# Kernel tuning notes

Hardware: AMD Instinct MI355X
Metric: run time of the kernel (lower is better)

## Reference

```python
import jax, jax.numpy as jnp
import numpy as np

EPS = 1e-5

def lrelu(x):
    return jnp.where(x > 0, x, 0.2 * x)

def bn(x, g, b, axes):
    # training-mode batch norm over `axes` (channel is last axis)
    m = jnp.mean(x, axis=axes, keepdims=True)
    v = jnp.var(x, axis=axes, keepdims=True)
    return g * (x - m) * jax.lax.rsqrt(v + EPS) + b

def knn_idx(x, k):
    # x: [B, N, C] -> idx of k nearest neighbors (incl. self): [B, N, k]
    xx = jnp.sum(x * x, axis=-1)                       # [B, N]
    inner = jnp.einsum('bnc,bmc->bnm', x, x)           # [B, N, N]
    neg_d = 2.0 * inner - xx[:, :, None] - xx[:, None, :]
    return jax.lax.top_k(neg_d, k)[1]

def graph_feature(x, k):
    # x: [B, N, C] -> edge features [B, N, k, 2C] = cat(x_j - x_i, x_i)
    idx = knn_idx(x, k)
    nb = jax.vmap(lambda xb, ib: xb[ib])(x, idx)       # [B, N, k, C]
    xc = jnp.broadcast_to(x[:, :, None, :], nb.shape)
    return jnp.concatenate([nb - xc, xc], axis=-1)

def edge_mlp(f, W, g, b):
    # 1x1 conv over edges + BN2d + LeakyReLU(0.2)
    h = jnp.einsum('bnkc,oc->bnko', f, W)
    return lrelu(bn(h, g, b, (0, 1, 2)))

def point_mlp(f, W, g, b):
    # 1x1 conv over points + BN1d + LeakyReLU(0.2)
    h = jnp.einsum('bnc,oc->bno', f, W)
    return lrelu(bn(h, g, b, (0, 1)))

def setup_inputs():
    key = jax.random.key(0)
    ks = jax.random.split(key, 16)
    B, N, K, E, C = 8, 4096, 20, 1024, 9
    inp = {'x': jax.random.normal(ks[0], (B, 3, N), jnp.float32), 'k': K}
    shapes = {'W1': (64, 6), 'W2': (64, 64), 'W3': (64, 128), 'W4': (64, 64),
              'W5': (64, 128), 'W6': (E, 192), 'W7': (512, 1216),
              'W8': (256, 512), 'W9': (C, 256)}
    for i, (n, s) in enumerate(shapes.items()):
        inp[n] = jax.random.normal(ks[i + 1], s, jnp.float32) * 0.05
    ch = [64, 64, 64, 64, 64, E, 512, 256]
    for i, c in enumerate(ch):
        inp['g%d' % (i + 1)] = jnp.ones((c,), jnp.float32)
        inp['b%d' % (i + 1)] = jnp.zeros((c,), jnp.float32)
    return inp

def reference(x, W1, W2, W3, W4, W5, W6, W7, W8, W9,
              g1, b1, g2, b2, g3, b3, g4, b4, g5, b5, g6, b6, g7, b7, g8, b8, k):
    xt = jnp.transpose(x, (0, 2, 1))                   # [B, N, 3]
    f = graph_feature(xt, k)                           # [B, N, k, 6]
    h = edge_mlp(f, W1, g1, b1)
    h = edge_mlp(h, W2, g2, b2)
    x1 = jnp.max(h, axis=2)                            # [B, N, 64]
    f = graph_feature(x1, k)                           # [B, N, k, 128]
    h = edge_mlp(f, W3, g3, b3)
    h = edge_mlp(h, W4, g4, b4)
    x2 = jnp.max(h, axis=2)                            # [B, N, 64]
    f = graph_feature(x2, k)
    h = edge_mlp(f, W5, g5, b5)
    x3 = jnp.max(h, axis=2)                            # [B, N, 64]
    cat = jnp.concatenate([x1, x2, x3], axis=-1)       # [B, N, 192]
    h6 = point_mlp(cat, W6, g6, b6)                    # [B, N, emb_dims]
    gmax = jnp.max(h6, axis=1, keepdims=True)          # global max pool
    gmax = jnp.broadcast_to(gmax, h6.shape)
    h = jnp.concatenate([gmax, x1, x2, x3], axis=-1)   # [B, N, 1216]
    h = point_mlp(h, W7, g7, b7)
    h = point_mlp(h, W8, g8, b8)
    # dropout is identity in eval mode
    out = jnp.einsum('bnc,oc->bno', h, W9)             # [B, N, num_classes]
    return out
```

## Files before the change

### kernel.cpp

```cpp
#include <hip/hip_runtime.h>
#include <hip/hip_bf16.h>

#define BB 8
#define NN 4096
#define KNN 20
#define NPTS (BB*NN)
#define NEDGE (NPTS*KNN)
#define TKCAP 12
#define LKN 12
#define SKN 24
#define FKN 48

typedef unsigned short u16;
typedef unsigned long long u64;
typedef __attribute__((ext_vector_type(8))) short s8v;
typedef __attribute__((ext_vector_type(4))) float f4v;

__device__ __forceinline__ float bf2f(u16 u) {
    return __uint_as_float(((unsigned)u) << 16);
}
__device__ __forceinline__ u16 f2bf_rne(float f) {
  unsigned u = __float_as_uint(f);
  unsigned rb = (u >> 16) & 1;
  u += 0x7FFFu + rb;
  return (u16)(u >> 16);
}
__device__ __forceinline__ float lrelu(float v) { return v > 0.f ? v : 0.2f * v; }
__device__ __forceinline__ double lrelu64(double v) { return v > 0.0 ? v : 0.2 * v; }

__device__ __forceinline__ u64 dkey(double v, int j) {
  u64 u = (u64)__double_as_longlong(v);
  u = (u >> 63) ? ~u : (u | 0x8000000000000000ull);
  return (u & ~0xFFFull) | (u64)(4095 - j);
}

__device__ __forceinline__ u64 skey(float v, int j) {
  unsigned s = __float_as_uint(v);
  s = (s >> 31) ? ~s : (s | 0x80000000u);
  return ((u64)s << 12) | (u64)(4095 - j);
}

template <int N>
__device__ __forceinline__ void tk_insert(u64* bk, u64 k) {
  if (k > bk[N - 1]) {
    bk[N - 1] = k;
#pragma unroll
    for (int p = N - 1; p > 0; --p) {
      if (bk[p] > bk[p - 1]) { u64 tv = bk[p]; bk[p] = bk[p - 1]; bk[p - 1] = tv; }
    }
  }
}

#define TOPK_INIT() \
  u64 bk[KNN]; \
  _Pragma("unroll") for (int p_ = 0; p_ < KNN; ++p_) bk[p_] = 0ull;

#define TOPK_INSERT(kk) do { \
    u64 k_ = (kk); \
    if (k_ > bk[KNN-1]) { \
      bk[KNN-1] = k_; \
      _Pragma("unroll") \
      for (int p_ = KNN-1; p_ > 0; --p_) { \
        if (bk[p_] > bk[p_-1]) { u64 tv_ = bk[p_]; bk[p_] = bk[p_-1]; bk[p_-1] = tv_; } \
      } \
    } \
  } while (0)

#define TKBUF_DECL() \
  u64 thr_ = 0ull; u64 cb_[TKCAP]; int cnt_ = 0;
#define TKBUF_PUSH(kk) do { \
    u64 k__ = (kk); \
    if (k__ > thr_) { cb_[cnt_] = k__; ++cnt_; } \
  } while (0)
#define TKBUF_FLUSH() do { \
    for (int l_ = 0; l_ < cnt_; ++l_) TOPK_INSERT(cb_[l_]); \
    cnt_ = 0; thr_ = bk[KNN-1]; \
  } while (0)

__global__ void det_k(const void* __restrict__ g1raw, int* __restrict__ flag) {
  const u16* u = (const u16*)g1raw;
  flag[0] = (u[0] == 0x3F80) ? 1 : 0;
}

__global__ __launch_bounds__(256) void conv_k(const void* __restrict__ src,
                                              float* __restrict__ dst, int n,
                                              const int* __restrict__ flag) {
  const int mode = flag[0];
  int i = blockIdx.x * 256 + threadIdx.x;
  const int stride = gridDim.x * 256;
  if (mode) {
    const u16* s = (const u16*)src;
    for (; i < n; i += stride) dst[i] = bf2f(s[i]);
  } else {
    const float* s = (const float*)src;
    for (; i < n; i += stride) dst[i] = s[i];
  }
}

__global__ void zero_k(double* __restrict__ p, int n) {
  int i = blockIdx.x * 256 + threadIdx.x;
  if (i < n) p[i] = 0.0;
}

__global__ __launch_bounds__(256) void knn1p_k(const float* __restrict__ x,
                                               u64* __restrict__ pkey) {
  __shared__ float sx[1024], sy[1024], sz[1024];
  __shared__ double sq[1024];
  const int b = blockIdx.x, t = threadIdx.x, seg = blockIdx.z;
  const int j0 = seg * 1024;
  const float* xb = x + b * 3 * NN;
  const int i = blockIdx.y * 256 + t;
// ... 343 lines not shown
  __syncthreads();
  if (t < 64) {
    double s = 0.0;
#pragma unroll
    for (int w = 0; w < 16; ++w) s += rPd[w][t];
    atomicAdd(&st[1024 + t], s);
  }
}

__global__ __launch_bounds__(256) void e1c_k(const float* __restrict__ x, const int* __restrict__ idx,
    const float* __restrict__ W1, const float* __restrict__ sc1, const float* __restrict__ sh1,
    const float* __restrict__ W2, const float* __restrict__ sc2, const float* __restrict__ sh2,
    float* __restrict__ x1out) {
  __shared__ float f6[80][9];
  __shared__ float h1s[80][68];
  const int t = threadIdx.x;
  const int p0 = blockIdx.x * 4;
  if (t < 80) {
    int e = p0 * KNN + t;
    int pt = e / KNN;
    int b = pt >> 12, i = pt & (NN - 1);
    int j = idx[e] & (NN - 1);
    const float* xb = x + b * 3 * NN;
    float xi0 = xb[i], xi1 = xb[NN + i], xi2 = xb[2 * NN + i];
    f6[t][0] = xb[j] - xi0; f6[t][1] = xb[NN + j] - xi1; f6[t][2] = xb[2 * NN + j] - xi2;
    f6[t][3] = xi0; f6[t][4] = xi1; f6[t][5] = xi2;
  }
  __syncthreads();
  const int c = t & 63;
  const int g4 = t >> 6;
  float w1[6];
#pragma unroll
  for (int d = 0; d < 6; ++d) w1[d] = W1[c * 6 + d];
  const float s1 = sc1[c], b1 = sh1[c];
  {
    float hk[20];
#pragma unroll
    for (int k = 0; k < 20; ++k) hk[k] = 0.f;
#pragma unroll
    for (int d = 0; d < 6; ++d) {
      float w1d = w1[d];
#pragma unroll
      for (int k = 0; k < 20; ++k) hk[k] = fmaf(f6[g4 + k * 4][d], w1d, hk[k]);
    }
#pragma unroll
    for (int k = 0; k < 20; ++k)
      h1s[g4 + k * 4][c] = lrelu(fmaf(s1, hk[k], b1));
  }
  __syncthreads();
  const float s2 = sc2[c], b2 = sh2[c];
  float acc[20];
#pragma unroll
  for (int k = 0; k < 20; ++k) acc[k] = 0.f;
  for (int d0 = 0; d0 < 64; d0 += 4) {
    float4 wv = *(const float4*)&W2[c * 64 + d0];
#pragma unroll
    for (int k = 0; k < 20; ++k) {
      float4 hv = *(const float4*)&h1s[g4 * 20 + k][d0];
      acc[k] = fmaf(hv.x, wv.x, acc[k]);
      acc[k] = fmaf(hv.y, wv.y, acc[k]);
      acc[k] = fmaf(hv.z, wv.z, acc[k]);
      acc[k] = fmaf(hv.w, wv.w, acc[k]);
    }
  }
  float m = -3.4e38f;
#pragma unroll
  for (int k = 0; k < 20; ++k) {
    float v = lrelu(fmaf(s2, acc[k], b2));
    m = fmaxf(m, v);
  }
  x1out[(p0 + g4) * 64 + c] = m;
}

__global__ void xx_k(const float* __restrict__ Xp, double* __restrict__ xx,
                     float* __restrict__ xxf) {
  const int row = blockIdx.x;
  float v = Xp[(size_t)row * 64 + threadIdx.x];
  double s = (double)v * (double)v;
#pragma unroll
  for (int o = 32; o > 0; o >>= 1) s += __shfl_down(s, o, 64);
  if (threadIdx.x == 0) { xx[row] = s; xxf[row] = (float)s; }
}

__global__ __launch_bounds__(256) void e2a_k(const float* __restrict__ xp,
                                             const int* __restrict__ idx,
                                             const float* __restrict__ W,
                                             double* __restrict__ st) {
  __shared__ float As[16][68];
  __shared__ float Ws[16][68];
  __shared__ double rPd[16][68];
  const int t = threadIdx.x;
  const int tx = t & 15, ty = t >> 4;
  const int lm = t >> 2, lk = (t & 3) * 4;
  double sL[4], qL[4];
#pragma unroll
  for (int j = 0; j < 4; ++j) { sL[j] = 0.0; qL[j] = 0.0; }
  for (int tile = 0; tile < 16; ++tile) {
    const int m0 = (blockIdx.x * 16 + tile) * 64;
    const int e = m0 + lm;
    const int grow = e / KNN;
    const int gj = ((grow >> 12) << 12) + (idx[e] & (NN - 1));
    float acc[4][4];
#pragma unroll
    for (int i = 0; i < 4; ++i)
#pragma unroll
      for (int j = 0; j < 4; ++j) acc[i][j] = 0.f;
    for (int k0 = 0; k0 < 128; k0 += 16) {
      const int c = k0 + lk;
      float4 a;
      if (c < 64) {
        float4 fj = *(const float4*)&xp[(size_t)gj * 64 + c];
        float4 fi = *(const float4*)&xp[(size_t)grow * 64 + c];
        a = make_float4(fj.x - fi.x, fj.y - fi.y, fj.z - fi.z, fj.w - fi.w);
      } else {
        a = *(const float4*)&xp[(size_t)grow * 64 + (c - 64)];
      }
      As[lk + 0][lm] = a.x; As[lk + 1][lm] = a.y;
      As[lk + 2][lm] = a.z; As[lk + 3][lm] = a.w;
      float4 wv = *(const float4*)&W[(size_t)lm * 128 + c];
      Ws[lk + 0][lm] = wv.x; Ws[lk + 1][lm] = wv.y;
      Ws[lk + 2][lm] = wv.z; Ws[lk + 3][lm] = wv.w;
      __syncthreads();
#pragma unroll
      for (int kk = 0; kk < 16; ++kk) {
        float4 a4 = *(const float4*)&As[kk][ty * 4];
        float4 b4 = *(const float4*)&Ws[kk][tx * 4];
        const float* aa = (const float*)&a4;
        const float* bb = (const float*)&b4;
#pragma unroll
        for (int i = 0; i < 4; ++i)
#pragma unroll
          for (int j = 0; j < 4; ++j)
            acc[i][j] = fmaf(aa[i], bb[j], acc[i][j]);
      }
      __syncthreads();
    }
#pragma unroll
    for (int j = 0; j < 4; ++j) {
      sL[j] += (double)acc[0][j] + (double)acc[1][j] + (double)acc[2][j] + (double)acc[3][j];
      qL[j] += (double)acc[0][j] * (double)acc[0][j] + (double)acc[1][j] * (double)acc[1][j]
             + (double)acc[2][j] * (double)acc[2][j] + (double)acc[3][j] * (double)acc[3][j];
    }
  }
#pragma unroll
  for (int j = 0; j < 4; ++j) rPd[ty][tx * 4 + j] = sL[j];
  __syncthreads();
  if (t < 64) {
    double s = 0.0;
#pragma unroll
    for (int w = 0; w < 16; ++w) s += rPd[w][t];
    atomicAdd(&st[t], s);
  }
  __syncthreads();
#pragma unroll
  for (int j = 0; j < 4; ++j) rPd[ty][tx * 4 + j] = qL[j];
  __syncthreads();
  if (t < 64) {
    double s = 0.0;
#pragma unroll
    for (int w = 0; w < 16; ++w) s += rPd[w][t];
    atomicAdd(&st[1024 + t], s);
  }
}

__global__ __launch_bounds__(256) void e2b_k(const float* __restrict__ xp,
    const int* __restrict__ idx, const float* __restrict__ W3,
    const float* __restrict__ sc3, const float* __restrict__ sh3,
    const float* __restrict__ W4, double* __restrict__ st) {
  __shared__ float As[16][68];
  __shared__ float Ws[16][68];
  __shared__ float H3[64][68];
  __shared__ float W4s[64][68];
  __shared__ double rPd[16][68];
  const int t = threadIdx.x;
  const int tx = t & 15, ty = t >> 4;
  const int lm = t >> 2, lk = (t & 3) * 4;
  for (int l = t; l < 4096; l += 256) W4s[l & 63][l >> 6] = W4[l];
  double sL[4], qL[4];
#pragma unroll
  for (int j = 0; j < 4; ++j) { sL[j] = 0.0; qL[j] = 0.0; }
  for (int tile = 0; tile < 16; ++tile) {
    const int m0 = (blockIdx.x * 16 + tile) * 64;
    const int e = m0 + lm;
    const int grow = e / KNN;
    const int gj = ((grow >> 12) << 12) + (idx[e] & (NN - 1));
    float acc1[4][4];
#pragma unroll
    for (int i = 0; i < 4; ++i)
#pragma unroll
      for (int j = 0; j < 4; ++j) acc1[i][j] = 0.f;
    for (int k0 = 0; k0 < 128; k0 += 16) {
      const int c = k0 + lk;
      float4 a;
      if (c < 64) {
        float4 fj = *(const float4*)&xp[(size_t)gj * 64 + c];
        float4 fi = *(const float4*)&xp[(size_t)grow * 64 + c];
        a = make_float4(fj.x - fi.x, fj.y - fi.y, fj.z - fi.z, fj.w - fi.w);
      } else {
        a = *(const float4*)&xp[(size_t)grow * 64 + (c - 64)];
      }
      As[lk + 0][lm] = a.x; As[lk + 1][lm] = a.y;
      As[lk + 2][lm] = a.z; As[lk + 3][lm] = a.w;
      float4 wv = *(const float4*)&W3[(size_t)lm * 128 + c];
      Ws[lk + 0][lm] = wv.x; Ws[lk + 1][lm] = wv.y;
      Ws[lk + 2][lm] = wv.z; Ws[lk + 3][lm] = wv.w;
      __syncthreads();
#pragma unroll
      for (int kk = 0; kk < 16; ++kk) {
        float4 a4 = *(const float4*)&As[kk][ty * 4];
        float4 b4 = *(const float4*)&Ws[kk][tx * 4];
        const float* aa = (const float*)&a4;
        const float* bb = (const float*)&b4;
#pragma unroll
        for (int i = 0; i < 4; ++i)
#pragma unroll
          for (int j = 0; j < 4; ++j)
            acc1[i][j] = fmaf(aa[i], bb[j], acc1[i][j]);
      }
      __syncthreads();
    }
#pragma unroll
    for (int j = 0; j < 4; ++j) {
      int c = tx * 4 + j;
      float s3 = sc3[c], b3 = sh3[c];
#pragma unroll
      for (int i = 0; i < 4; ++i)
        H3[c][ty * 4 + i] = lrelu(fmaf(s3, acc1[i][j], b3));
    }
    __syncthreads();
    float acc2[4][4];
#pragma unroll
    for (int i = 0; i < 4; ++i)
#pragma unroll
      for (int j = 0; j < 4; ++j) acc2[i][j] = 0.f;
    for (int k = 0; k < 64; ++k) {
      float4 a4 = *(const float4*)&H3[k][ty * 4];
      float4 b4 = *(const float4*)&W4s[k][tx * 4];
      const float* aa = (const float*)&a4;
      const float* bb = (const float*)&b4;
#pragma unroll
      for (int i = 0; i < 4; ++i)
#pragma unroll
        for (int j = 0; j < 4; ++j) acc2[i][j] = fmaf(aa[i], bb[j], acc2[i][j]);
    }
    __syncthreads();
#pragma unroll
    for (int j = 0; j < 4; ++j) {
      sL[j] += (double)acc2[0][j] + (double)acc2[1][j] + (double)acc2[2][j] + (double)acc2[3][j];
      qL[j] += (double)acc2[0][j] * (double)acc2[0][j] + (double)acc2[1][j] * (double)acc2[1][j]
             + (double)acc2[2][j] * (double)acc2[2][j] + (double)acc2[3][j] * (double)acc2[3][j];
    }
  }
#pragma unroll
  for (int j = 0; j < 4; ++j) rPd[ty][tx * 4 + j] = sL[j];
  __syncthreads();
  if (t < 64) {
    double s = 0.0;
#pragma unroll
    for (int w = 0; w < 16; ++w) s += rPd[w][t];
    atomicAdd(&st[t], s);
  }
  __syncthreads();
#pragma unroll
  for (int j = 0; j < 4; ++j) rPd[ty][tx * 4 + j] = qL[j];
  __syncthreads();
  if (t < 64) {
    double s = 0.0;
#pragma unroll
    for (int w = 0; w < 16; ++w) s += rPd[w][t];
    atomicAdd(&st[1024 + t], s);
  }
}

__global__ __launch_bounds__(256) void e2c_k(const float* __restrict__ xp,
    const int* __restrict__ idx, const float* __restrict__ W3,
    const float* __restrict__ sc3, const float* __restrict__ sh3,
    const float* __restrict__ W4, const float* __restrict__ sc4, const float* __restrict__ sh4,
    float* __restrict__ x2out) {
  __shared__ float fs[40][132];
  __shared__ float h3s[40][68];
  __shared__ float pmax[2][2][64];
  const int t = threadIdx.x;
  const int p0 = blockIdx.x * 2;
  for (int s = 0; s < 5; ++s) {
    int lin = s * 256 + t;
    int e = lin >> 5, v4 = lin & 31;
    int col = v4 * 4;
    int eg = p0 * KNN + e;
    int pt = p0 + e / KNN;
    int jr = ((pt >> 12) << 12) + (idx[eg] & (NN - 1));
    const float* xi = xp + (size_t)pt * 64;
    const float* xj = xp + (size_t)jr * 64;
    float4 a;
    if (col < 64) {
      float4 fj = *(const float4*)&xj[col];
      float4 fi = *(const float4*)&xi[col];
      a = make_float4(fj.x - fi.x, fj.y - fi.y, fj.z - fi.z, fj.w - fi.w);
    } else {
      a = *(const float4*)&xi[col - 64];
    }
    fs[e][col + 0] = a.x; fs[e][col + 1] = a.y; fs[e][col + 2] = a.z; fs[e][col + 3] = a.w;
  }
  __syncthreads();
  const int c = t & 63;
  const int g4 = t >> 6;
  const float s3 = sc3[c], b3 = sh3[c];
  {
    float hk[10];
#pragma unroll
    for (int k = 0; k < 10; ++k) hk[k] = 0.f;
    for (int d0 = 0; d0 < 128; d0 += 4) {
      float4 wv = *(const float4*)&W3[c * 128 + d0];
#pragma unroll
      for (int k = 0; k < 10; ++k) {
        float4 fv = *(const float4*)&fs[g4 + k * 4][d0];
        hk[k] = fmaf(fv.x, wv.x, hk[k]);
        hk[k] = fmaf(fv.y, wv.y, hk[k]);
        hk[k] = fmaf(fv.z, wv.z, hk[k]);
        hk[k] = fmaf(fv.w, wv.w, hk[k]);
      }
    }
#pragma unroll
    for (int k = 0; k < 10; ++k)
      h3s[g4 + k * 4][c] = lrelu(fmaf(s3, hk[k], b3));
  }
  __syncthreads();
  const int point = g4 & 1, khalf = g4 >> 1;
  const float s4 = sc4[c], b4 = sh4[c];
  float acc[10];
#pragma unroll
  for (int k = 0; k < 10; ++k) acc[k] = 0.f;
  for (int d0 = 0; d0 < 64; d0 += 4) {
    float4 wv = *(const float4*)&W4[c * 64 + d0];
#pragma unroll
    for (int k = 0; k < 10; ++k) {
      float4 hv = *(const float4*)&h3s[point * 20 + khalf * 10 + k][d0];
      acc[k] = fmaf(hv.x, wv.x, acc[k]);
      acc[k] = fmaf(hv.y, wv.y, acc[k]);
      acc[k] = fmaf(hv.z, wv.z, acc[k]);
      acc[k] = fmaf(hv.w, wv.w, acc[k]);
    }
  }
  float m = -3.4e38f;
#pragma unroll
  for (int k = 0; k < 10; ++k) {
    float v = lrelu(fmaf(s4, acc[k], b4));
    m = fmaxf(m, v);
  }
  pmax[khalf][point][c] = m;
  __syncthreads();
  if (t < 128) {
    int pp = t >> 6, cc = t & 63;
    x2out[(p0 + pp) * 64 + cc] = fmaxf(pmax[0][pp][cc], pmax[1][pp][cc]);
  }
}

__global__ __launch_bounds__(256) void e3c_k(const float* __restrict__ xp,
    const int* __restrict__ idx, const float* __restrict__ W5,
    const float* __restrict__ sc5, const float* __restrict__ sh5,
    float* __restrict__ x3out) {
  __shared__ float fs[80][132];
  const int t = threadIdx.x;
  const int p0 = blockIdx.x * 4;
  for (int s = 0; s < 10; ++s) {
    int lin = s * 256 + t;
    int e = lin >> 5, v4 = lin & 31;
    int col = v4 * 4;
    int eg = p0 * KNN + e;
    int pt = p0 + e / KNN;
    int jr = ((pt >> 12) << 12) + (idx[eg] & (NN - 1));
    const float* xi = xp + (size_t)pt * 64;
    const float* xj = xp + (size_t)jr * 64;
    float4 a;
    if (col < 64) {
      float4 fj = *(const float4*)&xj[col];
      float4 fi = *(const float4*)&xi[col];
      a = make_float4(fj.x - fi.x, fj.y - fi.y, fj.z - fi.z, fj.w - fi.w);
    } else {
      a = *(const float4*)&xi[col - 64];
    }
    fs[e][col + 0] = a.x; fs[e][col + 1] = a.y; fs[e][col + 2] = a.z; fs[e][col + 3] = a.w;
  }
  __syncthreads();
  const int c = t & 63;
  const int g4 = t >> 6;
  const float s5 = sc5[c], b5 = sh5[c];
  float acc[20];
#pragma unroll
  for (int k = 0; k < 20; ++k) acc[k] = 0.f;
  for (int d0 = 0; d0 < 128; d0 += 4) {
    float4 wv = *(const float4*)&W5[c * 128 + d0];
#pragma unroll
    for (int k = 0; k < 20; ++k) {
      float4 fv = *(const float4*)&fs[g4 * 20 + k][d0];
      acc[k] += fv.x * wv.x;
      acc[k] += fv.y * wv.y;
      acc[k] += fv.z * wv.z;
      acc[k] += fv.w * wv.w;
    }
  }
  float m = -3.4e38f;
#pragma unroll
  for (int k = 0; k < 20; ++k) m = fmaxf(m, lrelu(s5 * acc[k] + b5));
  x3out[(p0 + g4) * 64 + c] = m;
}

__global__ __launch_bounds__(256) void g6stats_k(
    const float* __restrict__ x1p, const float* __restrict__ x2p,
    const float* __restrict__ x3p, const float* __restrict__ W6,
    double* __restrict__ st, float* __restrict__ gpmax, float* __restrict__ gpmin) {
  __shared__ float As[16][68];
  __shared__ float Ws[16][68];
  __shared__ float rP[16][64];
  const int t = threadIdx.x;
  const int m0 = blockIdx.x * 64, n0 = blockIdx.y * 64;
  const int tx = t & 15, ty = t >> 4;
  const int lm = t >> 2, lk = (t & 3) * 4;
  const int m = m0 + lm, wn = n0 + lm;
  float acc[4][4];
#pragma unroll
  for (int i = 0; i < 4; ++i)
#pragma unroll
    for (int j = 0; j < 4; ++j) acc[i][j] = 0.f;
  for (int k0 = 0; k0 < 192; k0 += 16) {
    const int c = k0 + lk;
    const float* src = (c < 64)  ? &x1p[(size_t)m * 64 + c]
                     : (c < 128) ? &x2p[(size_t)m * 64 + (c - 64)]
                                 : &x3p[(size_t)m * 64 + (c - 128)];
    float4 av = *(const float4*)src;
    As[lk + 0][lm] = av.x; As[lk + 1][lm] = av.y;
    As[lk + 2][lm] = av.z; As[lk + 3][lm] = av.w;
    float4 wv = *(const float4*)&W6[(size_t)wn * 192 + c];
    Ws[lk + 0][lm] = wv.x; Ws[lk + 1][lm] = wv.y;
    Ws[lk + 2][lm] = wv.z; Ws[lk + 3][lm] = wv.w;
    __syncthreads();
#pragma unroll
    for (int kk = 0; kk < 16; ++kk) {
      float4 a4 = *(const float4*)&As[kk][ty * 4];
      float4 b4 = *(const float4*)&Ws[kk][tx * 4];
      const float* aa = (const float*)&a4;
      const float* bb = (const float*)&b4;
#pragma unroll
      for (int i = 0; i < 4; ++i)
#pragma unroll
        for (int j = 0; j < 4; ++j)
          acc[i][j] = fmaf(aa[i], bb[j], acc[i][j]);
    }
    __syncthreads();
  }
#pragma unroll
  for (int j = 0; j < 4; ++j)
    rP[ty][tx * 4 + j] = acc[0][j] + acc[1][j] + acc[2][j] + acc[3][j];
  __syncthreads();
  if (t < 64) {
    float ssum = 0.f;
#pragma unroll
    for (int w = 0; w < 16; ++w) ssum += rP[w][t];
    atomicAdd(&st[n0 + t], (double)ssum);
  }
  __syncthreads();
#pragma unroll
  for (int j = 0; j < 4; ++j)
    rP[ty][tx * 4 + j] = acc[0][j] * acc[0][j] + acc[1][j] * acc[1][j]
                       + acc[2][j] * acc[2][j] + acc[3][j] * acc[3][j];
  __syncthreads();
  if (t < 64) {
    float qsum = 0.f;
#pragma unroll
    for (int w = 0; w < 16; ++w) qsum += rP[w][t];
    atomicAdd(&st[1024 + n0 + t], (double)qsum);
  }
  __syncthreads();
#pragma unroll
  for (int j = 0; j < 4; ++j)
    rP[ty][tx * 4 + j] = fmaxf(fmaxf(acc[0][j], acc[1][j]), fmaxf(acc[2][j], acc[3][j]));
  __syncthreads();
  if (t < 64) {
    float mx = -3.4e38f;
#pragma unroll
    for (int w = 0; w < 16; ++w) mx = fmaxf(mx, rP[w][t]);
    gpmax[(size_t)blockIdx.x * 1024 + n0 + t] = mx;
  }
  __syncthreads();
#pragma unroll
  for (int j = 0; j < 4; ++j)
    rP[ty][tx * 4 + j] = fminf(fminf(acc[0][j], acc[1][j]), fminf(acc[2][j], acc[3][j]));
  __syncthreads();
// ... 278 lines not shown
      float4 wv = *(const float4*)&W8[(size_t)(n0 + lm) * 512 + c];
      Ws[lk + 0][lm] = wv.x; Ws[lk + 1][lm] = wv.y;
      Ws[lk + 2][lm] = wv.z; Ws[lk + 3][lm] = wv.w;
      __syncthreads();
#pragma unroll
      for (int kk = 0; kk < 16; ++kk) {
        float4 a4 = *(const float4*)&As[kk][ty * 4];
        float4 b4 = *(const float4*)&Ws[kk][tx * 4];
        const float* aa = (const float*)&a4;
        const float* bb = (const float*)&b4;
#pragma unroll
        for (int i = 0; i < 4; ++i)
#pragma unroll
          for (int j = 0; j < 4; ++j)
            acc[i][j] = fmaf(aa[i], bb[j], acc[i][j]);
      }
      __syncthreads();
    }
#pragma unroll
    for (int j = 0; j < 4; ++j) {
      int c = n0 + tx * 4 + j;
      float s8 = sc8[c], b8 = sh8[c];
#pragma unroll
      for (int i = 0; i < 4; ++i) {
        float v = lrelu(s8 * acc[i][j] + b8);
#pragma unroll
        for (int o = 0; o < 9; ++o) outp[i][o] += v * w9s[o][c];
      }
    }
  }
#pragma unroll
  for (int i = 0; i < 4; ++i)
#pragma unroll
    for (int o = 0; o < 9; ++o) rP[tx][(ty * 4 + i) * 9 + o] = outp[i][o];
  __syncthreads();
  const int mode = flag[0];
  for (int l = t; l < 576; l += 256) {
    float sum = 0.f;
#pragma unroll
    for (int w = 0; w < 16; ++w) sum += rP[w][l];
    if (mode) {
      ((__hip_bfloat16*)outp_raw)[(size_t)m0 * 9 + l] = __float2bfloat16(sum);
    } else {
      ((float*)outp_raw)[(size_t)m0 * 9 + l] = sum;
    }
  }
}

extern "C" void kernel_launch(void* const* d_in, const int* in_sizes, int n_in,
                              void* d_out, int out_size, void* d_ws, size_t ws_size,
                              hipStream_t stream) {
  (void)in_sizes; (void)out_size;
  if (n_in < 27) return;

  char* p = (char*)d_ws;
  size_t used = 0;
  auto alloc = [&](size_t bytes) {
    char* r = p;
    size_t rb = (bytes + 255) & ~(size_t)255;
    p += rb; used += rb;
    return r;
  };
  int* flag    = (int*)alloc(256);
  float* xF    = (float*)alloc((size_t)98304 * 4);
  float* W1f   = (float*)alloc((size_t)384 * 4);
  float* W2f   = (float*)alloc((size_t)4096 * 4);
  float* W3f   = (float*)alloc((size_t)8192 * 4);
  float* W4f   = (float*)alloc((size_t)4096 * 4);
  float* W5f   = (float*)alloc((size_t)8192 * 4);
  float* W6f   = (float*)alloc((size_t)196608 * 4);
  float* W7f   = (float*)alloc((size_t)622592 * 4);
  float* W8f   = (float*)alloc((size_t)131072 * 4);
  float* W9f   = (float*)alloc((size_t)2304 * 4);
  float* gF    = (float*)alloc((size_t)2112 * 4);
  float* bF    = (float*)alloc((size_t)2112 * 4);
  int* idxb    = (int*)alloc((size_t)NEDGE * 4);
  double* xx   = (double*)alloc((size_t)NPTS * 8);
  float* xxfb  = (float*)alloc((size_t)NPTS * 4);
  u16* Xhi     = (u16*)alloc((size_t)NPTS * 64 * 2);
  u16* Xlo     = (u16*)alloc((size_t)NPTS * 64 * 2);
  float* x1    = (float*)alloc((size_t)NPTS * 64 * 4);
  float* x2    = (float*)alloc((size_t)NPTS * 64 * 4);
  float* x3    = (float*)alloc((size_t)NPTS * 64 * 4);
  float* gm    = (float*)alloc((size_t)BB * 1024 * 4);
  float* gpmax = (float*)alloc((size_t)512 * 1024 * 4);
  float* gpmin = (float*)alloc((size_t)512 * 1024 * 4);
  float* gW    = (float*)alloc((size_t)4096 * 4);
  float* W7r   = (float*)alloc((size_t)98304 * 4);
  double* st   = (double*)alloc((size_t)2048 * 8);
  double* stm  = (double*)alloc((size_t)32 * 8);
  float* scb   = (float*)alloc((size_t)8 * 1024 * 4);
  float* shb   = (float*)alloc((size_t)8 * 1024 * 4);
  const int h7f32 = (ws_size >= used + (size_t)NPTS * 512 * 4 + 256) ? 1 : 0;
  void* h7 = alloc((size_t)NPTS * 512 * (h7f32 ? 4 : 2));
  if (ws_size < used) return;
  u64* pkey  = (u64*)h7;
  u64* pcand = (u64*)h7;

  det_k<<<1, 1, 0, stream>>>(d_in[11], flag);
  auto conv = [&](const void* src, float* dst, int n) {
    conv_k<<<(n + 255) / 256, 256, 0, stream>>>(src, dst, n, flag);
  };
  conv(d_in[0], xF, 98304);
  conv(d_in[2], W1f, 384);    conv(d_in[3], W2f, 4096);
  conv(d_in[4], W3f, 8192);   conv(d_in[5], W4f, 4096);
  conv(d_in[6], W5f, 8192);   conv(d_in[7], W6f, 196608);
  conv(d_in[8], W7f, 622592); conv(d_in[9], W8f, 131072);
  conv(d_in[10], W9f, 2304);
  const int gsz[8] = {64, 64, 64, 64, 64, 1024, 512, 256};
  int goff[8]; int acc_ = 0;
  for (int i = 0; i < 8; ++i) { goff[i] = acc_; acc_ += gsz[i]; }
  for (int i = 0; i < 8; ++i) {
    conv(d_in[11 + 2 * i], gF + goff[i], gsz[i]);
    conv(d_in[12 + 2 * i], bF + goff[i], gsz[i]);
  }
  wpack_k<<<384, 256, 0, stream>>>(W7f, W7r);
  auto SC = [&](int l) { return scb + (size_t)(l - 1) * 1024; };
  auto SH = [&](int l) { return shb + (size_t)(l - 1) * 1024; };
  auto G  = [&](int l) { return gF + goff[l - 1]; };
  auto Bt = [&](int l) { return bF + goff[l - 1]; };

  knn1p_k<<<dim3(BB, 16, 4), 256, 0, stream>>>(xF, pkey);
  tmerge_k<<<NPTS / 256, 256, 0, stream>>>(pkey, idxb);
  zero_k<<<1, 256, 0, stream>>>(stm, 32);
  f1mom_k<<<320, 256, 0, stream>>>(xF, idxb, stm);
  fin1_k<<<1, 64, 0, stream>>>(stm, W1f, G(1), Bt(1), SC(1), SH(1), 1.0 / NEDGE);
  zero_k<<<8, 256, 0, stream>>>(st, 2048);
  e1b_k<<<NEDGE / 1024, 256, 0, stream>>>(xF, idxb, W1f, SC(1), SH(1), W2f, st);
  fin_k<<<1, 256, 0, stream>>>(st, G(2), Bt(2), SC(2), SH(2), 64, 1.0 / NEDGE);
  e1c_k<<<NPTS / 4, 256, 0, stream>>>(xF, idxb, W1f, SC(1), SH(1), W2f, SC(2), SH(2), x1);

  xx_k<<<NPTS, 64, 0, stream>>>(x1, xx, xxfb);
  xsplit_k<<<NPTS * 64 / 256, 256, 0, stream>>>(x1, Xhi, Xlo);
  knnsm_k<<<dim3(NN / 16, BB), 256, 0, stream>>>(Xhi, Xlo, xxfb, pcand);
  resc_k<<<NPTS / 4, 256, 0, stream>>>(x1, xx, pcand, idxb);

  zero_k<<<8, 256, 0, stream>>>(st, 2048);
  e2a_k<<<NEDGE / 1024, 256, 0, stream>>>(x1, idxb, W3f, st);
  fin_k<<<1, 256, 0, stream>>>(st, G(3), Bt(3), SC(3), SH(3), 64, 1.0 / NEDGE);
  zero_k<<<8, 256, 0, stream>>>(st, 2048);
  e2b_k<<<NEDGE / 1024, 256, 0, stream>>>(x1, idxb, W3f, SC(3), SH(3), W4f, st);
  fin_k<<<1, 256, 0, stream>>>(st, G(4), Bt(4), SC(4), SH(4), 64, 1.0 / NEDGE);
  e2c_k<<<NPTS / 2, 256, 0, stream>>>(x1, idxb, W3f, SC(3), SH(3), W4f, SC(4), SH(4), x2);

  xx_k<<<NPTS, 64, 0, stream>>>(x2, xx, xxfb);
  xsplit_k<<<NPTS * 64 / 256, 256, 0, stream>>>(x2, Xhi, Xlo);
  knnsm_k<<<dim3(NN / 16, BB), 256, 0, stream>>>(Xhi, Xlo, xxfb, pcand);
  resc_k<<<NPTS / 4, 256, 0, stream>>>(x2, xx, pcand, idxb);

  zero_k<<<8, 256, 0, stream>>>(st, 2048);
  e2a_k<<<NEDGE / 1024, 256, 0, stream>>>(x2, idxb, W5f, st);
  fin_k<<<1, 256, 0, stream>>>(st, G(5), Bt(5), SC(5), SH(5), 64, 1.0 / NEDGE);
  e3c_k<<<NPTS / 4, 256, 0, stream>>>(x2, idxb, W5f, SC(5), SH(5), x3);

  zero_k<<<8, 256, 0, stream>>>(st, 2048);
  g6stats_k<<<dim3(NPTS / 64, 16), 256, 0, stream>>>(x1, x2, x3, W6f, st, gpmax, gpmin);
  fin_k<<<4, 256, 0, stream>>>(st, G(6), Bt(6), SC(6), SH(6), 1024, 1.0 / NPTS);
  gmax_red2_k<<<dim3(BB, 4), 256, 0, stream>>>(gpmax, gpmin, SC(6), SH(6), gm);

  gw_k<<<16, 256, 0, stream>>>(gm, W7f, gW);
  zero_k<<<8, 256, 0, stream>>>(st, 2048);
  if (h7f32) {
    g7stats_k<1><<<dim3(NPTS / 64, 8), 256, 0, stream>>>(x1, x2, x3, W7r, gW, h7, st);
  } else {
    g7stats_k<0><<<dim3(NPTS / 64, 8), 256, 0, stream>>>(x1, x2, x3, W7r, gW, h7, st);
  }
  fin_k<<<2, 256, 0, stream>>>(st, G(7), Bt(7), SC(7), SH(7), 512, 1.0 / NPTS);

  zero_k<<<8, 256, 0, stream>>>(st, 2048);
  if (h7f32) {
    gstats_k<4, 0, 1><<<dim3(NPTS / 64, 4), 256, 0, stream>>>(
        h7, W8f, 512, 256, nullptr, nullptr, nullptr, nullptr, SC(7), SH(7), nullptr, st);
  } else {
    gstats_k<4, 0, 0><<<dim3(NPTS / 64, 4), 256, 0, stream>>>(
        h7, W8f, 512, 256, nullptr, nullptr, nullptr, nullptr, SC(7), SH(7), nullptr, st);
  }
  fin_k<<<1, 256, 0, stream>>>(st, G(8), Bt(8), SC(8), SH(8), 256, 1.0 / NPTS);

  if (h7f32) {
    final_k<1><<<NPTS / 64, 256, 0, stream>>>(h7, SC(7), SH(7), W8f, SC(8), SH(8), W9f,
                                              d_out, flag);
  } else {
    final_k<0><<<NPTS / 64, 256, 0, stream>>>(h7, SC(7), SH(7), W8f, SC(8), SH(8), W9f,
                                              d_out, flag);
  }
}
```

Baseline: 3.781 ms.

## Factor edge conv as per-point GEMMs: W[:, :64]·x_j + (W[:, 64:]-W[:, :64])·x_i

```diff
diff --git a/kernel.cpp b/kernel.cpp
--- a/kernel.cpp
+++ b/kernel.cpp
@@ -26,7 +26,6 @@
   return (u16)(u >> 16);
 }
 __device__ __forceinline__ float lrelu(float v) { return v > 0.f ? v : 0.2f * v; }
-__device__ __forceinline__ double lrelu64(double v) { return v > 0.0 ? v : 0.2 * v; }
 
 __device__ __forceinline__ u64 dkey(double v, int j) {
   u64 u = (u64)__double_as_longlong(v);
@@ -536,150 +535,108 @@
   if (threadIdx.x == 0) { xx[row] = s; xxf[row] = (float)s; }
 }
 
-__global__ __launch_bounds__(256) void e2a_k(const float* __restrict__ xp,
-                                             const int* __restrict__ idx,
-                                             const float* __restrict__ W,
-                                             double* __restrict__ st) {
+__global__ void wd_k(const float* __restrict__ W, float* __restrict__ Wd) {
+  int i = blockIdx.x * 256 + threadIdx.x;
+  if (i < 4096) {
+    int c = i >> 6, d = i & 63;
+    Wd[i] = W[c * 128 + 64 + d] - W[c * 128 + d];
+  }
+}
+
+__global__ __launch_bounds__(256) void pgemm_k(const float* __restrict__ X,
+                                               const float* __restrict__ W, int ldw,
+                                               float* __restrict__ O) {
   __shared__ float As[16][68];
   __shared__ float Ws[16][68];
-  __shared__ double rPd[16][68];
   const int t = threadIdx.x;
+  const int m0 = blockIdx.x * 64;
   const int tx = t & 15, ty = t >> 4;
   const int lm = t >> 2, lk = (t & 3) * 4;
-  double sL[4], qL[4];
-#pragma unroll
-  for (int j = 0; j < 4; ++j) { sL[j] = 0.0; qL[j] = 0.0; }
-  for (int tile = 0; tile < 16; ++tile) {
-    const int m0 = (blockIdx.x * 16 + tile) * 64;
-    const int e = m0 + lm;
-    const int grow = e / KNN;
-    const int gj = ((grow >> 12) << 12) + (idx[e] & (NN - 1));
-    float acc[4][4];
-#pragma unroll
-    for (int i = 0; i < 4; ++i)
-#pragma unroll
-      for (int j = 0; j < 4; ++j) acc[i][j] = 0.f;
-    for (int k0 = 0; k0 < 128; k0 += 16) {
-      const int c = k0 + lk;
-      float4 a;
-      if (c < 64) {
-        float4 fj = *(const float4*)&xp[(size_t)gj * 64 + c];
-        float4 fi = *(const float4*)&xp[(size_t)grow * 64 + c];
-        a = make_float4(fj.x - fi.x, fj.y - fi.y, fj.z - fi.z, fj.w - fi.w);
-      } else {
-        a = *(const float4*)&xp[(size_t)grow * 64 + (c - 64)];
-      }
-      As[lk + 0][lm] = a.x; As[lk + 1][lm] = a.y;
-      As[lk + 2][lm] = a.z; As[lk + 3][lm] = a.w;
-      float4 wv = *(const float4*)&W[(size_t)lm * 128 + c];
-      Ws[lk + 0][lm] = wv.x; Ws[lk + 1][lm] = wv.y;
-      Ws[lk + 2][lm] = wv.z; Ws[lk + 3][lm] = wv.w;
-      __syncthreads();
-#pragma unroll
-      for (int kk = 0; kk < 16; ++kk) {
-        float4 a4 = *(const float4*)&As[kk][ty * 4];
-        float4 b4 = *(const float4*)&Ws[kk][tx * 4];
-        const float* aa = (const float*)&a4;
-        const float* bb = (const float*)&b4;
-#pragma unroll
-        for (int i = 0; i < 4; ++i)
-#pragma unroll
-          for (int j = 0; j < 4; ++j)
-            acc[i][j] = fmaf(aa[i], bb[j], acc[i][j]);
-      }
-      __syncthreads();
-    }
-#pragma unroll
-    for (int j = 0; j < 4; ++j) {
-      sL[j] += (double)acc[0][j] + (double)acc[1][j] + (double)acc[2][j] + (double)acc[3][j];
-      qL[j] += (double)acc[0][j] * (double)acc[0][j] + (double)acc[1][j] * (double)acc[1][j]
-             + (double)acc[2][j] * (double)acc[2][j] + (double)acc[3][j] * (double)acc[3][j];
-    }
-  }
-#pragma unroll
-  for (int j = 0; j < 4; ++j) rPd[ty][tx * 4 + j] = sL[j];
+  float acc[4][4];
+#pragma unroll
+  for (int i = 0; i < 4; ++i)
+#pragma unroll
+    for (int j = 0; j < 4; ++j) acc[i][j] = 0.f;
+  for (int k0 = 0; k0 < 64; k0 += 16) {
+    const int c = k0 + lk;
+    float4 av = *(const float4*)&X[(size_t)(m0 + lm) * 64 + c];
+    As[lk + 0][lm] = av.x; As[lk + 1][lm] = av.y;
+    As[lk + 2][lm] = av.z; As[lk + 3][lm] = av.w;
+    float4 wv = *(const float4*)&W[(size_t)lm * ldw + c];
+    Ws[lk + 0][lm] = wv.x; Ws[lk + 1][lm] = wv.y;
+    Ws[lk + 2][lm] = wv.z; Ws[lk + 3][lm] = wv.w;
+    __syncthreads();
+#pragma unroll
+    for (int kk = 0; kk < 16; ++kk) {
+      float4 a4 = *(const float4*)&As[kk][ty * 4];
+      float4 b4 = *(const float4*)&Ws[kk][tx * 4];
+      const float* aa = (const float*)&a4;
+      const float* bb = (const float*)&b4;
+#pragma unroll
+      for (int i = 0; i < 4; ++i)
+#pragma unroll
+        for (int j = 0; j < 4; ++j)
+          acc[i][j] = fmaf(aa[i], bb[j], acc[i][j]);
+    }
+    __syncthreads();
+  }
+#pragma unroll
+  for (int i = 0; i < 4; ++i)
+#pragma unroll
+    for (int j = 0; j < 4; ++j)
+      O[(size_t)(m0 + ty * 4 + i) * 64 + tx * 4 + j] = acc[i][j];
+}
+
+__global__ __launch_bounds__(256) void eastats_k(const float* __restrict__ A,
+                                                 const float* __restrict__ Bm,
+                                                 const int* __restrict__ idx,
+                                                 double* __restrict__ st) {
+  __shared__ double rs[4][64], rq[4][64];
+  const int t = threadIdx.x;
+  const int c = t & 63, g4 = t >> 6;
+  const int e0 = blockIdx.x * 2048;
+  double s = 0.0, q = 0.0;
+  for (int e = e0 + g4; e < e0 + 2048; e += 4) {
+    int pt = e / KNN;
+    int j = ((pt >> 12) << 12) + (idx[e] & (NN - 1));
+    float v = A[(size_t)j * 64 + c] + Bm[(size_t)pt * 64 + c];
+    s += (double)v;
+    q += (double)v * (double)v;
+  }
+  rs[g4][c] = s; rq[g4][c] = q;
   __syncthreads();
   if (t < 64) {
-    double s = 0.0;
-#pragma unroll
-    for (int w = 0; w < 16; ++w) s += rPd[w][t];
-    atomicAdd(&st[t], s);
-  }
-  __syncthreads();
-#pragma unroll
-  for (int j = 0; j < 4; ++j) rPd[ty][tx * 4 + j] = qL[j];
-  __syncthreads();
-  if (t < 64) {
-    double s = 0.0;
-#pragma unroll
-    for (int w = 0; w < 16; ++w) s += rPd[w][t];
-    atomicAdd(&st[1024 + t], s);
-  }
-}
-
-__global__ __launch_bounds__(256) void e2b_k(const float* __restrict__ xp,
-    const int* __restrict__ idx, const float* __restrict__ W3,
+    double ss = rs[0][t] + rs[1][t] + rs[2][t] + rs[3][t];
+    double qq = rq[0][t] + rq[1][t] + rq[2][t] + rq[3][t];
+    atomicAdd(&st[t], ss);
+    atomicAdd(&st[1024 + t], qq);
+  }
+}
+
+__global__ __launch_bounds__(256) void ebstats_k(const float* __restrict__ A,
+    const float* __restrict__ Bm, const int* __restrict__ idx,
     const float* __restrict__ sc3, const float* __restrict__ sh3,
     const float* __restrict__ W4, double* __restrict__ st) {
-  __shared__ float As[16][68];
-  __shared__ float Ws[16][68];
   __shared__ float H3[64][68];
   __shared__ float W4s[64][68];
   __shared__ double rPd[16][68];
   const int t = threadIdx.x;
   const int tx = t & 15, ty = t >> 4;
-  const int lm = t >> 2, lk = (t & 3) * 4;
+  const int c = t & 63, g4 = t >> 6;
   for (int l = t; l < 4096; l += 256) W4s[l & 63][l >> 6] = W4[l];
+  const float s3 = sc3[c], b3 = sh3[c];
   double sL[4], qL[4];
 #pragma unroll
   for (int j = 0; j < 4; ++j) { sL[j] = 0.0; qL[j] = 0.0; }
   for (int tile = 0; tile < 16; ++tile) {
-    const int m0 = (blockIdx.x * 16 + tile) * 64;
-    const int e = m0 + lm;
-    const int grow = e / KNN;
-    const int gj = ((grow >> 12) << 12) + (idx[e] & (NN - 1));
-    float acc1[4][4];
-#pragma unroll
-    for (int i = 0; i < 4; ++i)
-#pragma unroll
-      for (int j = 0; j < 4; ++j) acc1[i][j] = 0.f;
-    for (int k0 = 0; k0 < 128; k0 += 16) {
-      const int c = k0 + lk;
-      float4 a;
-      if (c < 64) {
-        float4 fj = *(const float4*)&xp[(size_t)gj * 64 + c];
-        float4 fi = *(const float4*)&xp[(size_t)grow * 64 + c];
-        a = make_float4(fj.x - fi.x, fj.y - fi.y, fj.z - fi.z, fj.w - fi.w);
-      } else {
-        a = *(const float4*)&xp[(size_t)grow * 64 + (c - 64)];
-      }
-      As[lk + 0][lm] = a.x; As[lk + 1][lm] = a.y;
-      As[lk + 2][lm] = a.z; As[lk + 3][lm] = a.w;
-      float4 wv = *(const float4*)&W3[(size_t)lm * 128 + c];
-      Ws[lk + 0][lm] = wv.x; Ws[lk + 1][lm] = wv.y;
-      Ws[lk + 2][lm] = wv.z; Ws[lk + 3][lm] = wv.w;
-      __syncthreads();
-#pragma unroll
-      for (int kk = 0; kk < 16; ++kk) {
-        float4 a4 = *(const float4*)&As[kk][ty * 4];
-        float4 b4 = *(const float4*)&Ws[kk][tx * 4];
-        const float* aa = (const float*)&a4;
-        const float* bb = (const float*)&b4;
-#pragma unroll
-        for (int i = 0; i < 4; ++i)
-#pragma unroll
-          for (int j = 0; j < 4; ++j)
-            acc1[i][j] = fmaf(aa[i], bb[j], acc1[i][j]);
-      }
-      __syncthreads();
-    }
-#pragma unroll
-    for (int j = 0; j < 4; ++j) {
-      int c = tx * 4 + j;
-      float s3 = sc3[c], b3 = sh3[c];
-#pragma unroll
-      for (int i = 0; i < 4; ++i)
-        H3[c][ty * 4 + i] = lrelu(fmaf(s3, acc1[i][j], b3));
+    const int e0 = (blockIdx.x * 16 + tile) * 64;
+    __syncthreads();
+    for (int es = g4; es < 64; es += 4) {
+      int e = e0 + es;
+      int pt = e / KNN;
+      int j = ((pt >> 12) << 12) + (idx[e] & (NN - 1));
+      float v = A[(size_t)j * 64 + c] + Bm[(size_t)pt * 64 + c];
+      H3[c][es] = lrelu(fmaf(s3, v, b3));
     }
     __syncthreads();
     float acc2[4][4];
@@ -697,7 +654,6 @@
 #pragma unroll
         for (int j = 0; j < 4; ++j) acc2[i][j] = fmaf(aa[i], bb[j], acc2[i][j]);
     }
-    __syncthreads();
 #pragma unroll
     for (int j = 0; j < 4; ++j) {
       sL[j] += (double)acc2[0][j] + (double)acc2[1][j] + (double)acc2[2][j] + (double)acc2[3][j];
@@ -705,6 +661,7 @@
              + (double)acc2[2][j] * (double)acc2[2][j] + (double)acc2[3][j] * (double)acc2[3][j];
     }
   }
+  __syncthreads();
 #pragma unroll
   for (int j = 0; j < 4; ++j) rPd[ty][tx * 4 + j] = sL[j];
   __syncthreads();
@@ -726,57 +683,24 @@
   }
 }
 
-__global__ __launch_bounds__(256) void e2c_k(const float* __restrict__ xp,
-    const int* __restrict__ idx, const float* __restrict__ W3,
+__global__ __launch_bounds__(256) void e2c_k(const float* __restrict__ A,
+    const float* __restrict__ Bm, const int* __restrict__ idx,
     const float* __restrict__ sc3, const float* __restrict__ sh3,
     const float* __restrict__ W4, const float* __restrict__ sc4, const float* __restrict__ sh4,
     float* __restrict__ x2out) {
-  __shared__ float fs[40][132];
   __shared__ float h3s[40][68];
   __shared__ float pmax[2][2][64];
   const int t = threadIdx.x;
   const int p0 = blockIdx.x * 2;
-  for (int s = 0; s < 5; ++s) {
-    int lin = s * 256 + t;
-    int e = lin >> 5, v4 = lin & 31;
-    int col = v4 * 4;
-    int eg = p0 * KNN + e;
-    int pt = p0 + e / KNN;
-    int jr = ((pt >> 12) << 12) + (idx[eg] & (NN - 1));
-    const float* xi = xp + (size_t)pt * 64;
-    const float* xj = xp + (size_t)jr * 64;
-    float4 a;
-    if (col < 64) {
-      float4 fj = *(const float4*)&xj[col];
-      float4 fi = *(const float4*)&xi[col];
-      a = make_float4(fj.x - fi.x, fj.y - fi.y, fj.z - fi.z, fj.w - fi.w);
-    } else {
-      a = *(const float4*)&xi[col - 64];
-    }
-    fs[e][col + 0] = a.x; fs[e][col + 1] = a.y; fs[e][col + 2] = a.z; fs[e][col + 3] = a.w;
-  }
-  __syncthreads();
   const int c = t & 63;
   const int g4 = t >> 6;
   const float s3 = sc3[c], b3 = sh3[c];
-  {
-    float hk[10];
-#pragma unroll
-    for (int k = 0; k < 10; ++k) hk[k] = 0.f;
-    for (int d0 = 0; d0 < 128; d0 += 4) {
-      float4 wv = *(const float4*)&W3[c * 128 + d0];
-#pragma unroll
-      for (int k = 0; k < 10; ++k) {
-        float4 fv = *(const float4*)&fs[g4 + k * 4][d0];
-        hk[k] = fmaf(fv.x, wv.x, hk[k]);
-        hk[k] = fmaf(fv.y, wv.y, hk[k]);
-        hk[k] = fmaf(fv.z, wv.z, hk[k]);
-        hk[k] = fmaf(fv.w, wv.w, hk[k]);
-      }
-    }
-#pragma unroll
-    for (int k = 0; k < 10; ++k)
-      h3s[g4 + k * 4][c] = lrelu(fmaf(s3, hk[k], b3));
+  for (int es = g4; es < 40; es += 4) {
+    int eg = p0 * KNN + es;
+    int pt = p0 + es / KNN;
+    int jr = ((pt >> 12) << 12) + (idx[eg] & (NN - 1));
+    float v = A[(size_t)jr * 64 + c] + Bm[(size_t)pt * 64 + c];
+    h3s[es][c] = lrelu(fmaf(s3, v, b3));
   }
   __syncthreads();
   const int point = g4 & 1, khalf = g4 >> 1;
@@ -809,54 +733,26 @@
   }
 }
 
-__global__ __launch_bounds__(256) void e3c_k(const float* __restrict__ xp,
-    const int* __restrict__ idx, const float* __restrict__ W5,
+__global__ __launch_bounds__(256) void e3c_k(const float* __restrict__ A,
+    const float* __restrict__ Bm, const int* __restrict__ idx,
     const float* __restrict__ sc5, const float* __restrict__ sh5,
     float* __restrict__ x3out) {
-  __shared__ float fs[80][132];
   const int t = threadIdx.x;
   const int p0 = blockIdx.x * 4;
-  for (int s = 0; s < 10; ++s) {
-    int lin = s * 256 + t;
-    int e = lin >> 5, v4 = lin & 31;
-    int col = v4 * 4;
-    int eg = p0 * KNN + e;
-    int pt = p0 + e / KNN;
-    int jr = ((pt >> 12) << 12) + (idx[eg] & (NN - 1));
-    const float* xi = xp + (size_t)pt * 64;
-    const float* xj = xp + (size_t)jr * 64;
-    float4 a;
-    if (col < 64) {
-      float4 fj = *(const float4*)&xj[col];
-      float4 fi = *(const float4*)&xi[col];
-      a = make_float4(fj.x - fi.x, fj.y - fi.y, fj.z - fi.z, fj.w - fi.w);
-    } else {
-      a = *(const float4*)&xi[col - 64];
-    }
-    fs[e][col + 0] = a.x; fs[e][col + 1] = a.y; fs[e][col + 2] = a.z; fs[e][col + 3] = a.w;
-  }
-  __syncthreads();
-  const int c = t & 63;
-  const int g4 = t >> 6;
+  const int c = t & 63, g4 = t >> 6;
+  const int pt = p0 + g4;
   const float s5 = sc5[c], b5 = sh5[c];
-  float acc[20];
-#pragma unroll
-  for (int k = 0; k < 20; ++k) acc[k] = 0.f;
-  for (int d0 = 0; d0 < 128; d0 += 4) {
-    float4 wv = *(const float4*)&W5[c * 128 + d0];
-#pragma unroll
-    for (int k = 0; k < 20; ++k) {
-      float4 fv = *(const float4*)&fs[g4 * 20 + k][d0];
-      acc[k] += fv.x * wv.x;
-      acc[k] += fv.y * wv.y;
-      acc[k] += fv.z * wv.z;
-      acc[k] += fv.w * wv.w;
-    }
-  }
+  const float bb = Bm[(size_t)pt * 64 + c];
+  const int* ip = idx + (size_t)pt * KNN;
+  const int bbase = (pt >> 12) << 12;
   float m = -3.4e38f;
-#pragma unroll
-  for (int k = 0; k < 20; ++k) m = fmaxf(m, lrelu(s5 * acc[k] + b5));
-  x3out[(p0 + g4) * 64 + c] = m;
+#pragma unroll 4
+  for (int k = 0; k < KNN; ++k) {
+    int jr = bbase + (ip[k] & (NN - 1));
+    float v = A[(size_t)jr * 64 + c] + bb;
+    m = fmaxf(m, lrelu(fmaf(s5, v, b5)));
+  }
+  x3out[(size_t)pt * 64 + c] = m;
 }
 
 __global__ __launch_bounds__(256) void g6stats_k(
@@ -1301,6 +1197,9 @@
   float* x1    = (float*)alloc((size_t)NPTS * 64 * 4);
   float* x2    = (float*)alloc((size_t)NPTS * 64 * 4);
   float* x3    = (float*)alloc((size_t)NPTS * 64 * 4);
+  float* Ab    = (float*)alloc((size_t)NPTS * 64 * 4);
+  float* Bb    = (float*)alloc((size_t)NPTS * 64 * 4);
+  float* Wd    = (float*)alloc((size_t)4096 * 4);
   float* gm    = (float*)alloc((size_t)BB * 1024 * 4);
   float* gpmax = (float*)alloc((size_t)512 * 1024 * 4);
   float* gpmin = (float*)alloc((size_t)512 * 1024 * 4);
@@ -1354,23 +1253,29 @@
   knnsm_k<<<dim3(NN / 16, BB), 256, 0, stream>>>(Xhi, Xlo, xxfb, pcand);
   resc_k<<<NPTS / 4, 256, 0, stream>>>(x1, xx, pcand, idxb);
 
+  wd_k<<<16, 256, 0, stream>>>(W3f, Wd);
+  pgemm_k<<<NPTS / 64, 256, 0, stream>>>(x1, W3f, 128, Ab);
+  pgemm_k<<<NPTS / 64, 256, 0, stream>>>(x1, Wd, 64, Bb);
   zero_k<<<8, 256, 0, stream>>>(st, 2048);
-  e2a_k<<<NEDGE / 1024, 256, 0, stream>>>(x1, idxb, W3f, st);
+  eastats_k<<<NEDGE / 2048, 256, 0, stream>>>(Ab, Bb, idxb, st);
   fin_k<<<1, 256, 0, stream>>>(st, G(3), Bt(3), SC(3), SH(3), 64, 1.0 / NEDGE);
   zero_k<<<8, 256, 0, stream>>>(st, 2048);
-  e2b_k<<<NEDGE / 1024, 256, 0, stream>>>(x1, idxb, W3f, SC(3), SH(3), W4f, st);
+  ebstats_k<<<NEDGE / 1024, 256, 0, stream>>>(Ab, Bb, idxb, SC(3), SH(3), W4f, st);
   fin_k<<<1, 256, 0, stream>>>(st, G(4), Bt(4), SC(4), SH(4), 64, 1.0 / NEDGE);
-  e2c_k<<<NPTS / 2, 256, 0, stream>>>(x1, idxb, W3f, SC(3), SH(3), W4f, SC(4), SH(4), x2);
+  e2c_k<<<NPTS / 2, 256, 0, stream>>>(Ab, Bb, idxb, SC(3), SH(3), W4f, SC(4), SH(4), x2);
 
   xx_k<<<NPTS, 64, 0, stream>>>(x2, xx, xxfb);
   xsplit_k<<<NPTS * 64 / 256, 256, 0, stream>>>(x2, Xhi, Xlo);
   knnsm_k<<<dim3(NN / 16, BB), 256, 0, stream>>>(Xhi, Xlo, xxfb, pcand);
   resc_k<<<NPTS / 4, 256, 0, stream>>>(x2, xx, pcand, idxb);
 
+  wd_k<<<16, 256, 0, stream>>>(W5f, Wd);
+  pgemm_k<<<NPTS / 64, 256, 0, stream>>>(x2, W5f, 128, Ab);
+  pgemm_k<<<NPTS / 64, 256, 0, stream>>>(x2, Wd, 64, Bb);
   zero_k<<<8, 256, 0, stream>>>(st, 2048);
-  e2a_k<<<NEDGE / 1024, 256, 0, stream>>>(x2, idxb, W5f, st);
+  eastats_k<<<NEDGE / 2048, 256, 0, stream>>>(Ab, Bb, idxb, st);
   fin_k<<<1, 256, 0, stream>>>(st, G(5), Bt(5), SC(5), SH(5), 64, 1.0 / NEDGE);
-  e3c_k<<<NPTS / 4, 256, 0, stream>>>(x2, idxb, W5f, SC(5), SH(5), x3);
+  e3c_k<<<NPTS / 4, 256, 0, stream>>>(Ab, Bb, idxb, SC(5), SH(5), x3);
 
   zero_k<<<8, 256, 0, stream>>>(st, 2048);
   g6stats_k<<<dim3(NPTS / 64, 16), 256, 0, stream>>>(x1, x2, x3, W6f, st, gpmax, gpmin);
```

Result: faster. 3.332 ms (-11.9%).
